# Performance work log

Hardware: AMD Instinct MI355X
Metric: run time of the kernel (lower is better)

## Reference

```python
import jax, jax.numpy as jnp
import numpy as np

N = 100000   # nodes
R = 4        # relations
E = 160000   # edges per relation
DIN = 128
DOUT = 128


def setup_inputs() -> dict:
    key = jax.random.key(0)
    k = jax.random.split(key, 5)
    x = jax.random.normal(k[0], (N, DIN), dtype=jnp.float32)
    src = jax.random.randint(k[1], (R, E), 0, N, dtype=jnp.int32)
    dst = jax.random.randint(k[2], (R, E), 0, N, dtype=jnp.int32)
    # per-relation weights (Linear.weight.T in the original), xavier-ish scale
    W = jax.random.normal(k[3], (R, DIN, DOUT), dtype=jnp.float32) / np.sqrt(DIN)
    Wl = jax.random.normal(k[4], (DIN, DOUT), dtype=jnp.float32) / np.sqrt(DIN)
    b = jnp.zeros((DOUT,), dtype=jnp.float32)
    return {"x": x, "W": W, "Wl": Wl, "b": b, "src": src, "dst": dst}


def reference(x, W, Wl, b, src, dst):
    # DGL GraphConv(norm='right', in==out): aggregate messages first, then matmul.
    def per_rel(s, d):
        agg = jax.ops.segment_sum(x[s], d, num_segments=N)          # [N, DIN]
        deg = jax.ops.segment_sum(jnp.ones(s.shape, x.dtype), d, num_segments=N)
        return agg / jnp.clip(deg, 1.0)[:, None]                     # right norm

    aggs = jax.vmap(per_rel)(src, dst)            # [R, N, DIN]
    h = jnp.einsum('rnd,rde->ne', aggs, W)        # per-relation GEMM + sum over relations
    h = h + x @ Wl + b                            # self-loop Linear with bias
    return jax.nn.relu(h)                         # activation; dropout p=0.0 is identity
```

## Files before the change

kernel.cpp:

```cpp
#include <hip/hip_runtime.h>

#define DIN 128
#define DOUT 128

typedef float f4 __attribute__((ext_vector_type(4)));
typedef float f32x4 __attribute__((ext_vector_type(4)));
typedef short bf16x8 __attribute__((ext_vector_type(8)));
typedef unsigned short u16x8 __attribute__((ext_vector_type(8)));
typedef unsigned short u16x4 __attribute__((ext_vector_type(4)));

__device__ inline unsigned short f2bf(float f) {
    unsigned u = __float_as_uint(f);
    u += 0x7FFFu + ((u >> 16) & 1u);
    return (unsigned short)(u >> 16);
}

__global__ void preamble(const float* __restrict__ W, const float* __restrict__ Wl,
                         const float* __restrict__ x, const int* __restrict__ dst,
                         unsigned short* __restrict__ Wt, unsigned short* __restrict__ xbf,
                         int* __restrict__ cnt,
                         int nbW, int nbX, int E, int N, int totE) {
    const int b = blockIdx.x;
    const int t = threadIdx.x;
    if (b < nbW) {
        int id = b * 256 + t;
        if (id >= 5 * DIN * DOUT) return;
        int m    = id >> 14;
        int rem  = id & 16383;
        int din  = rem >> 7;
        int dout = rem & 127;
        float v = (m < 4) ? W[(m << 14) + din * DOUT + dout] : Wl[din * DOUT + dout];
        Wt[(m << 14) + dout * DIN + din] = f2bf(v);
    } else if (b < nbW + nbX) {
        int tid = (b - nbW) * 256 + t;
        if (tid >= N * 16) return;
        const float* xr = x + (long long)tid * 8;
        f4 lo = *(const f4*)xr;
        f4 hi = *(const f4*)(xr + 4);
        u16x8 p;
        p[0] = f2bf(lo[0]); p[1] = f2bf(lo[1]); p[2] = f2bf(lo[2]); p[3] = f2bf(lo[3]);
        p[4] = f2bf(hi[0]); p[5] = f2bf(hi[1]); p[6] = f2bf(hi[2]); p[7] = f2bf(hi[3]);
        *(u16x8*)&xbf[(long long)tid * 8] = p;
    } else {
        int i = (b - nbW - nbX) * 256 + t;
        if (i >= totE) return;
        int r = i / E;
        atomicAdd(&cnt[r * N + dst[i]], 1);
    }
}

__global__ void scan1(const int* __restrict__ cnt, int* __restrict__ off,
                      int* __restrict__ part, int M) {
    __shared__ int sd[256];
    const int t = threadIdx.x, b = blockIdx.x;
    const int base = b * 2048 + t * 8;
    int v[8]; int tsum = 0;
    #pragma unroll
    for (int i = 0; i < 8; i++) { int g = base + i; v[i] = (g < M) ? cnt[g] : 0; tsum += v[i]; }
    sd[t] = tsum; __syncthreads();
    for (int d = 1; d < 256; d <<= 1) {
        int val = 0;
        if (t >= d) val = sd[t - d];
        __syncthreads();
        if (t >= d) sd[t] += val;
        __syncthreads();
    }
    int run = sd[t] - tsum;
    if (t == 255) part[b] = sd[255];
    #pragma unroll
    for (int i = 0; i < 8; i++) { int g = base + i; if (g < M) off[g] = run; run += v[i]; }
}

__global__ void scan2(int* __restrict__ part, int nb, int* __restrict__ offM) {
    __shared__ int sd[256];
    const int t = threadIdx.x;
    int v = (t < nb) ? part[t] : 0;
    sd[t] = v; __syncthreads();
    for (int d = 1; d < 256; d <<= 1) {
        int val = 0;
        if (t >= d) val = sd[t - d];
        __syncthreads();
        if (t >= d) sd[t] += val;
        __syncthreads();
    }
    if (t < nb) part[t] = sd[t] - v;
    if (t == 255) *offM = sd[255];
}

__global__ void scan3(int* __restrict__ off, const int* __restrict__ part, int M) {
    const int add = part[blockIdx.x];
    const int base = blockIdx.x * 2048 + threadIdx.x;
    #pragma unroll
    for (int i = 0; i < 8; i++) { int g = base + i * 256; if (g < M) off[g] += add; }
}

__global__ void fill_csr(const int* __restrict__ src, const int* __restrict__ dst,
                         const int* __restrict__ off, int* __restrict__ cnt,
                         int* __restrict__ csr, int E, int N, int total) {
    int i = blockIdx.x * 256 + threadIdx.x;
    if (i >= total) return;
    int r = i / E;
    int idx = r * N + dst[i];
    int pos = atomicAdd(&cnt[idx], -1) - 1;
    csr[off[idx] + pos] = src[i];
}

__global__ __launch_bounds__(256)
void gather_bf(const unsigned short* __restrict__ xbf, const int* __restrict__ off,
               const int* __restrict__ csr, unsigned short* __restrict__ agg,
               int N, int total) {
    int tid = blockIdx.x * 256 + threadIdx.x;
    if (tid >= total) return;
    const int c  = tid & 15;
    const int nn = tid >> 4;
    const int n  = nn % N;
    const int rr = nn / N;

    const int idx = rr * N + n;
    const int s0 = off[idx];
    const int s1 = off[idx + 1];

    float acc[8];
    #pragma unroll
    for (int i = 0; i < 8; i++) acc[i] = 0.0f;

    for (int e = s0; e < s1; e++) {
        const int s = csr[e];
        u16x8 v = *(const u16x8*)&xbf[(long long)s * DIN + c * 8];
        #pragma unroll
        for (int i = 0; i < 8; i++)
            acc[i] += __uint_as_float(((unsigned)v[i]) << 16);
    }
    const float sc = 1.0f / fmaxf((float)(s1 - s0), 1.0f);
    u16x8 p;
    #pragma unroll
    for (int i = 0; i < 8; i++) p[i] = f2bf(acc[i] * sc);
    *(u16x8*)&agg[((long long)rr * N + n) * DIN + c * 8] = p;
}

__global__ __launch_bounds__(256)
void gather_f32(const float* __restrict__ x, const int* __restrict__ off,
                const int* __restrict__ csr, unsigned short* __restrict__ agg,
                int r0, int N, int total) {
    int tid = blockIdx.x * 256 + threadIdx.x;
    if (tid >= total) return;
    const int c  = tid & 31;
    const int nn = tid >> 5;
    const int n  = nn % N;
    const int rr = nn / N;

    const int idx = (r0 + rr) * N + n;
    const int s0 = off[idx];
    const int s1 = off[idx + 1];

    f4 acc = (f4)(0.0f);
    for (int e = s0; e < s1; e++) {
        const int s = csr[e];
        acc += *(const f4*)&x[(long long)s * DIN + c * 4];
    }
    const float sc = 1.0f / fmaxf((float)(s1 - s0), 1.0f);
    acc *= sc;

    u16x4 p;
    p[0] = f2bf(acc[0]); p[1] = f2bf(acc[1]);
    p[2] = f2bf(acc[2]); p[3] = f2bf(acc[3]);
    *(u16x4*)&agg[((long long)rr * N + n) * DIN + c * 4] = p;
}

__global__ __launch_bounds__(512, 2)
void gemm_lds(const unsigned short* __restrict__ agg,
              const unsigned short* __restrict__ xbf,
              const unsigned short* __restrict__ Wt,
              const float* __restrict__ bias,
              float* __restrict__ out, int N) {
    __shared__ unsigned short Ws[128 * 128];

    const int t    = threadIdx.x;
    const int lane = t & 63;
    const int w    = t >> 6;
    const int n0   = blockIdx.x * 128;
    const int lr   = lane & 15;
    const int kg   = lane >> 4;
    const int lrm  = lr & 7;

    const int rowA = n0 + w * 16 + lr;
    const int rowC = (rowA < N) ? rowA : (N - 1);

    const long long relStride = (long long)N * DIN;

    f32x4 acc[8];
    #pragma unroll
    for (int ct = 0; ct < 8; ct++) acc[ct] = (f32x4)(0.0f);

    const unsigned short* aSrc0 = agg + (long long)rowC * DIN;

    bf16x8 aCur[4], aNxt[4];
    #pragma unroll
    for (int k = 0; k < 4; k++)
        aCur[k] = *(const bf16x8*)&aSrc0[k * 32 + kg * 8];

    for (int r = 0; r < 5; r++) {
        {
            const unsigned short* Wg = Wt + ((long long)r << 14);
            u16x8 tmp[4];
            #pragma unroll
            for (int p = 0; p < 4; p++) {
                const int li = t + p * 512;
                tmp[p] = *(const u16x8*)&Wg[((li >> 4) << 7) + (li & 15) * 8];
            }
            #pragma unroll
            for (int p = 0; p < 4; p++) {
                const int li  = t + p * 512;
                const int row = li >> 4, cg = li & 15;
                *(u16x8*)&Ws[(row << 7) + ((cg ^ (row & 7)) << 3)] = tmp[p];
            }
        }
        if (r < 4) {
            const unsigned short* an = (r < 3)
                ? agg + (r + 1) * relStride + (long long)rowC * DIN
                : xbf + (long long)rowC * DIN;
            #pragma unroll
            for (int k = 0; k < 4; k++)
                aNxt[k] = *(const bf16x8*)&an[k * 32 + kg * 8];
        }
        __syncthreads();

        #pragma unroll
        for (int k0i = 0; k0i < 4; k0i++) {
            #pragma unroll
            for (int ct = 0; ct < 8; ct++) {
                const int row  = ct * 16 + lr;
                const int slot = (k0i * 4 + kg) ^ lrm;
                bf16x8 b = *(const bf16x8*)&Ws[(row << 7) + (slot << 3)];
                acc[ct] = __builtin_amdgcn_mfma_f32_16x16x32_bf16(aCur[k0i], b, acc[ct], 0, 0, 0);
            }
        }
        if (r < 4) {
            #pragma unroll
            for (int k = 0; k < 4; k++) aCur[k] = aNxt[k];
            __syncthreads();
        }
    }

    #pragma unroll
    for (int j = 0; j < 4; j++) {
        int n2 = n0 + w * 16 + kg * 4 + j;
        if (n2 >= N) continue;
        float* orow = out + (long long)n2 * DOUT + lr;
        #pragma unroll
        for (int ct = 0; ct < 8; ct++) {
            float v = acc[ct][j] + bias[ct * 16 + lr];
            orow[ct * 16] = fmaxf(v, 0.0f);
        }
    }
}

__global__ __launch_bounds__(256, 4)
void gemm_direct(const float* __restrict__ x, const unsigned short* __restrict__ agg,
                 const unsigned short* __restrict__ Wt, const float* __restrict__ bias,
                 float* __restrict__ out, int N, int relStart, int nRel,
                 int doSelf, int accumulate) {
    const int t    = threadIdx.x;
    const int lane = t & 63;
    const int w    = t >> 6;
    const int n0   = blockIdx.x * 64;
    const int lr   = lane & 15;
    const int kg   = lane >> 4;

    const int rowA = n0 + w * 16 + lr;
    const int rowC = (rowA < N) ? rowA : (N - 1);

    f32x4 acc[8];
    #pragma unroll
    for (int ct = 0; ct < 8; ct++) acc[ct] = (f32x4)(0.0f);

    for (int rr = 0; rr < nRel; rr++) {
        const unsigned short* aggR = agg + ((long long)rr * N + rowC) * DIN;
        const unsigned short* WtR  = Wt + ((long long)(relStart + rr) << 14);
        #pragma unroll
        for (int k0 = 0; k0 < DIN; k0 += 32) {
            bf16x8 a = *(const bf16x8*)&aggR[k0 + kg * 8];
            #pragma unroll
            for (int ct = 0; ct < 8; ct++) {
                bf16x8 bfr = *(const bf16x8*)&WtR[((ct * 16 + lr) << 7) + k0 + kg * 8];
                acc[ct] = __builtin_amdgcn_mfma_f32_16x16x32_bf16(a, bfr, acc[ct], 0, 0, 0);
            }
        }
    }

    if (doSelf) {
        const float* xr = x + (long long)rowC * DIN;
        const unsigned short* WtS = Wt + ((long long)4 << 14);
        #pragma unroll
        for (int k0 = 0; k0 < DIN; k0 += 32) {
            f4 v  = *(const f4*)(xr + k0 + kg * 8);
            f4 v2 = *(const f4*)(xr + k0 + kg * 8 + 4);
            bf16x8 a;
            a[0] = (short)f2bf(v[0]);  a[1] = (short)f2bf(v[1]);
            a[2] = (short)f2bf(v[2]);  a[3] = (short)f2bf(v[3]);
            a[4] = (short)f2bf(v2[0]); a[5] = (short)f2bf(v2[1]);
            a[6] = (short)f2bf(v2[2]); a[7] = (short)f2bf(v2[3]);
            #pragma unroll
            for (int ct = 0; ct < 8; ct++) {
                bf16x8 bfr = *(const bf16x8*)&WtS[((ct * 16 + lr) << 7) + k0 + kg * 8];
                acc[ct] = __builtin_amdgcn_mfma_f32_16x16x32_bf16(a, bfr, acc[ct], 0, 0, 0);
            }
        }
    }

    #pragma unroll
    for (int j = 0; j < 4; j++) {
        int n2 = n0 + w * 16 + kg * 4 + j;
        if (n2 >= N) continue;
        float* orow = out + (long long)n2 * DOUT + lr;
        #pragma unroll
        for (int ct = 0; ct < 8; ct++) {
            float v = acc[ct][j];
            if (accumulate) v += orow[ct * 16];
            if (doSelf) {
                v += bias[ct * 16 + lr];
                v = fmaxf(v, 0.0f);
            }
            orow[ct * 16] = v;
        }
    }
}

extern "C" void kernel_launch(void* const* d_in, const int* in_sizes, int n_in,
                              void* d_out, int out_size, void* d_ws, size_t ws_size,
                              hipStream_t stream) {
    const float* x  = (const float*)d_in[0];
    const float* W  = (const float*)d_in[1];
    const float* Wl = (const float*)d_in[2];
    const float* b  = (const float*)d_in[3];
    const int* src  = (const int*)d_in[4];
    const int* dst  = (const int*)d_in[5];
    float* out = (float*)d_out;

    const int N = in_sizes[0] / DIN;
    const int R = in_sizes[1] / (DIN * DOUT);
    const int E = in_sizes[4] / R;
    const int M = R * N;
    const int totE = R * E;

    char* wsp = (char*)d_ws;
    unsigned short* Wt = (unsigned short*)wsp;
    int* cnt  = (int*)(wsp + 5 * 16384 * 2);
    int* off  = cnt + M;
    int* part = off + M + 1;
    int* csr  = part + 256;
    size_t preBytes = ((char*)(csr + totE) - wsp + 255) & ~(size_t)255;
    unsigned short* agg = (unsigned short*)(wsp + preBytes);
    const size_t aggBytes = (size_t)N * DIN * sizeof(unsigned short);
    const bool pathA = (ws_size >= preBytes + 5 * aggBytes) && (R == 4);

    hipMemsetAsync(cnt, 0, (size_t)M * sizeof(int), stream);

    const int nb = (M + 2047) / 2048;

    if (pathA) {
        unsigned short* xbf = agg + 4 * (size_t)N * DIN;

        const int nbW = (5 * DIN * DOUT + 255) / 256;
        const int nbX = (N * 16 + 255) / 256;
        const int nbD = (totE + 255) / 256;
        preamble<<<nbW + nbX + nbD, 256, 0, stream>>>(W, Wl, x, dst, Wt, xbf, cnt,
                                                      nbW, nbX, E, N, totE);

        scan1<<<nb, 256, 0, stream>>>(cnt, off, part, M);
        scan2<<<1, 256, 0, stream>>>(part, nb, off + M);
        scan3<<<nb, 256, 0, stream>>>(off, part, M);
        fill_csr<<<(totE + 255) / 256, 256, 0, stream>>>(src, dst, off, cnt, csr, E, N, totE);

        const int total = R * N * 16;
        gather_bf<<<(total + 255) / 256, 256, 0, stream>>>(xbf, off, csr, agg, N, total);

        gemm_lds<<<(N + 127) / 128, 512, 0, stream>>>(agg, xbf, Wt, b, out, N);
    } else {
        const int nbW = (5 * DIN * DOUT + 255) / 256;
        const int nbD = (totE + 255) / 256;
        preamble<<<nbW + nbD, 256, 0, stream>>>(W, Wl, x, dst, Wt, nullptr, cnt,
                                                nbW, 0, E, N, totE);
        scan1<<<nb, 256, 0, stream>>>(cnt, off, part, M);
        scan2<<<1, 256, 0, stream>>>(part, nb, off + M);
        scan3<<<nb, 256, 0, stream>>>(off, part, M);
        fill_csr<<<(totE + 255) / 256, 256, 0, stream>>>(src, dst, off, cnt, csr, E, N, totE);

        const int total = N * 32;
        const int gemmGrid = (N + 63) / 64;
        for (int r = 0; r < R; r++) {
            gather_f32<<<(total + 255) / 256, 256, 0, stream>>>(x, off, csr, agg, r, N, total);
            gemm_direct<<<gemmGrid, 256, 0, stream>>>(x, agg, Wt, b, out, N,
                                                      r, 1, (r == R - 1),
                                                      (r > 0));
        }
    }
}
```

Before: 174.6 us.

## Drop scan3 by folding block offsets into consumers; double-buffer GEMM weight tiles

Removes the third scan kernel. fill_csr and the gather kernels now add the per-block prefix (part[idx>>11]) on the fly, and the total is stored at part[nb]. In gemm_lds the weight tile moves to a two-slot LDS buffer, so the next relation's weights are loaded from global memory during the current MFMA loop and written to the other slot afterwards. This drops one __syncthreads per relation and one kernel launch, at the cost of an extra part[] load per lookup and twice the LDS (64KB), which may limit occupancy at launch_bounds(512,2).

After: 168.5 us. 1.04x faster.

```diff
diff --git a/kernel.cpp b/kernel.cpp
--- a/kernel.cpp
+++ b/kernel.cpp
@@ -71,7 +71,7 @@
     for (int i = 0; i < 8; i++) { int g = base + i; if (g < M) off[g] = run; run += v[i]; }
 }
 
-__global__ void scan2(int* __restrict__ part, int nb, int* __restrict__ offM) {
+__global__ void scan2(int* __restrict__ part, int nb) {
     __shared__ int sd[256];
     const int t = threadIdx.x;
     int v = (t < nb) ? part[t] : 0;
@@ -84,31 +84,25 @@
         __syncthreads();
     }
     if (t < nb) part[t] = sd[t] - v;
-    if (t == 255) *offM = sd[255];
-}
-
-__global__ void scan3(int* __restrict__ off, const int* __restrict__ part, int M) {
-    const int add = part[blockIdx.x];
-    const int base = blockIdx.x * 2048 + threadIdx.x;
-    #pragma unroll
-    for (int i = 0; i < 8; i++) { int g = base + i * 256; if (g < M) off[g] += add; }
+    if (t == 255) part[nb] = sd[255];
 }
 
 __global__ void fill_csr(const int* __restrict__ src, const int* __restrict__ dst,
-                         const int* __restrict__ off, int* __restrict__ cnt,
-                         int* __restrict__ csr, int E, int N, int total) {
+                         const int* __restrict__ off, const int* __restrict__ part,
+                         int* __restrict__ cnt, int* __restrict__ csr,
+                         int E, int N, int total) {
     int i = blockIdx.x * 256 + threadIdx.x;
     if (i >= total) return;
     int r = i / E;
     int idx = r * N + dst[i];
     int pos = atomicAdd(&cnt[idx], -1) - 1;
-    csr[off[idx] + pos] = src[i];
+    csr[off[idx] + part[idx >> 11] + pos] = src[i];
 }
 
 __global__ __launch_bounds__(256)
 void gather_bf(const unsigned short* __restrict__ xbf, const int* __restrict__ off,
-               const int* __restrict__ csr, unsigned short* __restrict__ agg,
-               int N, int total) {
+               const int* __restrict__ part, const int* __restrict__ csr,
+               unsigned short* __restrict__ agg, int N, int M, int total) {
     int tid = blockIdx.x * 256 + threadIdx.x;
     if (tid >= total) return;
     const int c  = tid & 15;
@@ -117,8 +111,9 @@
     const int rr = nn / N;
 
     const int idx = rr * N + n;
-    const int s0 = off[idx];
-    const int s1 = off[idx + 1];
+    const int s0 = off[idx] + part[idx >> 11];
+    const int i1 = idx + 1;
+    const int s1 = (i1 < M) ? (off[i1] + part[i1 >> 11]) : part[(M + 2047) >> 11];
 
     float acc[8];
     #pragma unroll
@@ -140,8 +135,8 @@
 
 __global__ __launch_bounds__(256)
 void gather_f32(const float* __restrict__ x, const int* __restrict__ off,
-                const int* __restrict__ csr, unsigned short* __restrict__ agg,
-                int r0, int N, int total) {
+                const int* __restrict__ part, const int* __restrict__ csr,
+                unsigned short* __restrict__ agg, int r0, int N, int M, int total) {
     int tid = blockIdx.x * 256 + threadIdx.x;
     if (tid >= total) return;
     const int c  = tid & 31;
@@ -150,8 +145,9 @@
     const int rr = nn / N;
 
     const int idx = (r0 + rr) * N + n;
-    const int s0 = off[idx];
-    const int s1 = off[idx + 1];
+    const int s0 = off[idx] + part[idx >> 11];
+    const int i1 = idx + 1;
+    const int s1 = (i1 < M) ? (off[i1] + part[i1 >> 11]) : part[(M + 2047) >> 11];
 
     f4 acc = (f4)(0.0f);
     for (int e = s0; e < s1; e++) {
@@ -173,7 +169,7 @@
               const unsigned short* __restrict__ Wt,
               const float* __restrict__ bias,
               float* __restrict__ out, int N) {
-    __shared__ unsigned short Ws[128 * 128];
+    __shared__ unsigned short Ws[2][128 * 128];
 
     const int t    = threadIdx.x;
     const int lane = t & 63;
@@ -185,37 +181,39 @@
 
     const int rowA = n0 + w * 16 + lr;
     const int rowC = (rowA < N) ? rowA : (N - 1);
-
     const long long relStride = (long long)N * DIN;
 
     f32x4 acc[8];
     #pragma unroll
     for (int ct = 0; ct < 8; ct++) acc[ct] = (f32x4)(0.0f);
 
-    const unsigned short* aSrc0 = agg + (long long)rowC * DIN;
+    int sRow[4], sCg[4];
+    #pragma unroll
+    for (int p = 0; p < 4; p++) { const int li = t + p * 512; sRow[p] = li >> 4; sCg[p] = li & 15; }
+
+    u16x8 tmp[4];
+    #pragma unroll
+    for (int p = 0; p < 4; p++)
+        tmp[p] = *(const u16x8*)&Wt[(sRow[p] << 7) + sCg[p] * 8];
 
     bf16x8 aCur[4], aNxt[4];
-    #pragma unroll
-    for (int k = 0; k < 4; k++)
-        aCur[k] = *(const bf16x8*)&aSrc0[k * 32 + kg * 8];
+    {
+        const unsigned short* a0 = agg + (long long)rowC * DIN;
+        #pragma unroll
+        for (int k = 0; k < 4; k++)
+            aCur[k] = *(const bf16x8*)&a0[k * 32 + kg * 8];
+    }
+    #pragma unroll
+    for (int p = 0; p < 4; p++)
+        *(u16x8*)&Ws[0][(sRow[p] << 7) + ((sCg[p] ^ (sRow[p] & 7)) << 3)] = tmp[p];
+    __syncthreads();
 
     for (int r = 0; r < 5; r++) {
-        {
-            const unsigned short* Wg = Wt + ((long long)r << 14);
-            u16x8 tmp[4];
-            #pragma unroll
-            for (int p = 0; p < 4; p++) {
-                const int li = t + p * 512;
-                tmp[p] = *(const u16x8*)&Wg[((li >> 4) << 7) + (li & 15) * 8];
-            }
-            #pragma unroll
-            for (int p = 0; p < 4; p++) {
-                const int li  = t + p * 512;
-                const int row = li >> 4, cg = li & 15;
-                *(u16x8*)&Ws[(row << 7) + ((cg ^ (row & 7)) << 3)] = tmp[p];
-            }
-        }
         if (r < 4) {
+            const unsigned short* Wg = Wt + ((long long)(r + 1) << 14);
+            #pragma unroll
+            for (int p = 0; p < 4; p++)
+                tmp[p] = *(const u16x8*)&Wg[(sRow[p] << 7) + sCg[p] * 8];
             const unsigned short* an = (r < 3)
                 ? agg + (r + 1) * relStride + (long long)rowC * DIN
                 : xbf + (long long)rowC * DIN;
@@ -223,19 +221,23 @@
             for (int k = 0; k < 4; k++)
                 aNxt[k] = *(const bf16x8*)&an[k * 32 + kg * 8];
         }
-        __syncthreads();
-
+
+        const unsigned short* Wb = Ws[r & 1];
         #pragma unroll
         for (int k0i = 0; k0i < 4; k0i++) {
             #pragma unroll
             for (int ct = 0; ct < 8; ct++) {
                 const int row  = ct * 16 + lr;
                 const int slot = (k0i * 4 + kg) ^ lrm;
-                bf16x8 b = *(const bf16x8*)&Ws[(row << 7) + (slot << 3)];
+                bf16x8 b = *(const bf16x8*)&Wb[(row << 7) + (slot << 3)];
                 acc[ct] = __builtin_amdgcn_mfma_f32_16x16x32_bf16(aCur[k0i], b, acc[ct], 0, 0, 0);
             }
         }
+
         if (r < 4) {
+            #pragma unroll
+            for (int p = 0; p < 4; p++)
+                *(u16x8*)&Ws[(r + 1) & 1][(sRow[p] << 7) + ((sCg[p] ^ (sRow[p] & 7)) << 3)] = tmp[p];
             #pragma unroll
             for (int k = 0; k < 4; k++) aCur[k] = aNxt[k];
             __syncthreads();
@@ -348,7 +350,7 @@
     int* cnt  = (int*)(wsp + 5 * 16384 * 2);
     int* off  = cnt + M;
     int* part = off + M + 1;
-    int* csr  = part + 256;
+    int* csr  = part + 260;
     size_t preBytes = ((char*)(csr + totE) - wsp + 255) & ~(size_t)255;
     unsigned short* agg = (unsigned short*)(wsp + preBytes);
     const size_t aggBytes = (size_t)N * DIN * sizeof(unsigned short);
@@ -368,12 +370,13 @@
                                                       nbW, nbX, E, N, totE);
 
         scan1<<<nb, 256, 0, stream>>>(cnt, off, part, M);
-        scan2<<<1, 256, 0, stream>>>(part, nb, off + M);
-        scan3<<<nb, 256, 0, stream>>>(off, part, M);
-        fill_csr<<<(totE + 255) / 256, 256, 0, stream>>>(src, dst, off, cnt, csr, E, N, totE);
+        scan2<<<1, 256, 0, stream>>>(part, nb);
+        fill_csr<<<(totE + 255) / 256, 256, 0, stream>>>(src, dst, off, part, cnt, csr,
+                                                         E, N, totE);
 
         const int total = R * N * 16;
-        gather_bf<<<(total + 255) / 256, 256, 0, stream>>>(xbf, off, csr, agg, N, total);
+        gather_bf<<<(total + 255) / 256, 256, 0, stream>>>(xbf, off, part, csr, agg,
+                                                           N, M, total);
 
         gemm_lds<<<(N + 127) / 128, 512, 0, stream>>>(agg, xbf, Wt, b, out, N);
     } else {
@@ -382,14 +385,15 @@
         preamble<<<nbW + nbD, 256, 0, stream>>>(W, Wl, x, dst, Wt, nullptr, cnt,
                                                 nbW, 0, E, N, totE);
         scan1<<<nb, 256, 0, stream>>>(cnt, off, part, M);
-        scan2<<<1, 256, 0, stream>>>(part, nb, off + M);
-        scan3<<<nb, 256, 0, stream>>>(off, part, M);
-        fill_csr<<<(totE + 255) / 256, 256, 0, stream>>>(src, dst, off, cnt, csr, E, N, totE);
+        scan2<<<1, 256, 0, stream>>>(part, nb);
+        fill_csr<<<(totE + 255) / 256, 256, 0, stream>>>(src, dst, off, part, cnt, csr,
+                                                         E, N, totE);
 
         const int total = N * 32;
         const int gemmGrid = (N + 63) / 64;
         for (int r = 0; r < R; r++) {
-            gather_f32<<<(total + 255) / 256, 256, 0, stream>>>(x, off, csr, agg, r, N, total);
+            gather_f32<<<(total + 255) / 256, 256, 0, stream>>>(x, off, part, csr, agg,
+                                                                r, N, M, total);
             gemm_direct<<<gemmGrid, 256, 0, stream>>>(x, agg, Wt, b, out, N,
                                                       r, 1, (r == R - 1),
                                                       (r > 0));
```
